# Performance work log

Hardware: AMD Instinct MI355X
Metric: run time of the kernel (lower is better)

Reference implementation:

```python
import jax, jax.numpy as jnp
import numpy as np
import math

D_MODEL = 96
D_STATE = 16
D_CONV = 3
D_INNER = 192          # expand=2 * d_model
DT_RANK = 6            # ceil(96/16)
K = 4                  # scan directions
B, H, W = 1, 64, 64


def setup_inputs() -> dict:
    key = jax.random.key(0)
    ks = jax.random.split(key, 10)
    x = jax.random.normal(ks[0], (B, H, W, D_MODEL), dtype=jnp.float32)
    in_proj_w = jax.random.normal(ks[1], (2 * D_INNER, D_MODEL), jnp.float32) / np.sqrt(D_MODEL)
    conv_w = jax.random.normal(ks[2], (D_CONV, D_CONV, 1, D_INNER), jnp.float32) * 0.1  # HWIO depthwise
    conv_b = jax.random.normal(ks[3], (D_INNER,), jnp.float32) * 0.01
    x_proj_w = jax.random.normal(ks[4], (K, DT_RANK + 2 * D_STATE, D_INNER), jnp.float32) / np.sqrt(D_INNER)
    dt_std = DT_RANK ** -0.5
    dt_w = jax.random.uniform(ks[5], (K, D_INNER, DT_RANK), jnp.float32, -dt_std, dt_std)
    # faithful dt bias init: dt ~ exp(U*(log(dt_max)-log(dt_min))+log(dt_min)), inverse-softplus
    dt = jnp.exp(jax.random.uniform(ks[6], (K, D_INNER), jnp.float32) * (math.log(0.1) - math.log(0.001)) + math.log(0.001))
    dt = jnp.clip(dt, 1e-4, None)
    dt_b = dt + jnp.log(-jnp.expm1(-dt))
    A_logs = jnp.tile(jnp.log(jnp.arange(1, D_STATE + 1, dtype=jnp.float32))[None, :], (K * D_INNER, 1))
    Ds = jnp.ones((K * D_INNER,), jnp.float32)
    ln_g = jnp.ones((D_INNER,), jnp.float32)
    ln_b = jnp.zeros((D_INNER,), jnp.float32)
    out_w = jax.random.normal(ks[7], (D_MODEL, D_INNER), jnp.float32) / np.sqrt(D_INNER)
    return dict(x=x, in_proj_w=in_proj_w, conv_w=conv_w, conv_b=conv_b, x_proj_w=x_proj_w,
                dt_w=dt_w, dt_b=dt_b, A_logs=A_logs, Ds=Ds, ln_g=ln_g, ln_b=ln_b, out_w=out_w)


def _silu(v):
    return v * jax.nn.sigmoid(v)


def _ss2d(x, in_proj_w, conv_w, conv_b, x_proj_w, dt_w, dt_b, A_logs, Ds, ln_g, ln_b, out_w):
    b, h, w, _ = x.shape
    L = h * w
    # in_proj, split x/z
    xz = jnp.einsum('bhwc,oc->bhwo', x, in_proj_w)
    x_, z = jnp.split(xz, 2, axis=-1)                              # (B,H,W,Di) each
    # depthwise 3x3 conv (SAME) + SiLU, NHWC
    xc = jax.lax.conv_general_dilated(x_, conv_w, (1, 1), 'SAME',
                                      dimension_numbers=('NHWC', 'HWIO', 'NHWC'),
                                      feature_group_count=D_INNER) + conv_b
    xc = _silu(xc)
    xd = xc.transpose(0, 3, 1, 2)                                   # (B,Di,H,W)
    x_row = xd.reshape(b, D_INNER, L)
    x_col = xd.transpose(0, 1, 3, 2).reshape(b, D_INNER, L)
    x_hwwh = jnp.stack([x_row, x_col], axis=1)                      # (B,2,Di,L)
    xs = jnp.concatenate([x_hwwh, jnp.flip(x_hwwh, axis=-1)], axis=1)  # (B,K,Di,L)
    # projections for dt / B / C
    x_dbl = jnp.einsum('bkdl,kcd->bkcl', xs, x_proj_w)
    dts = x_dbl[:, :, :DT_RANK]
    Bs = x_dbl[:, :, DT_RANK:DT_RANK + D_STATE]                     # (B,K,N,L)
    Cs = x_dbl[:, :, DT_RANK + D_STATE:]                            # (B,K,N,L)
    dts = jnp.einsum('bkrl,kdr->bkdl', dts, dt_w)
    delta = jax.nn.softplus(dts + dt_b[None, :, :, None])           # (B,K,Di,L)
    A = -jnp.exp(A_logs).reshape(K, D_INNER, D_STATE)
    # selective scan: h_l = exp(delta_l*A) h_{l-1} + delta_l*B_l*u_l ; y_l = C_l . h_l + D*u_l
    dA = jnp.exp(delta[..., None] * A[None, :, :, None, :])         # (B,K,Di,L,N)
    Bt = Bs.transpose(0, 1, 3, 2)                                   # (B,K,L,N)
    dBu = delta[..., None] * Bt[:, :, None] * xs[..., None]         # (B,K,Di,L,N)

    def comb(e1, e2):
        a1, b1 = e1
        a2, b2 = e2
        return a1 * a2, a2 * b1 + b2

    _, hstate = jax.lax.associative_scan(comb, (dA, dBu), axis=3)
    Ct = Cs.transpose(0, 1, 3, 2)                                   # (B,K,L,N)
    out_y = jnp.einsum('bkdln,bkln->bkdl', hstate, Ct) + Ds.reshape(K, D_INNER)[None, :, :, None] * xs
    y = out_y.sum(1).reshape(b, D_INNER, h, w).transpose(0, 2, 3, 1)  # (B,H,W,Di)
    # LayerNorm over channels
    mu = y.mean(-1, keepdims=True)
    var = y.var(-1, keepdims=True)
    y = (y - mu) * jax.lax.rsqrt(var + 1e-5) * ln_g + ln_b
    y = y * _silu(z)
    return jnp.einsum('bhwd,od->bhwo', y, out_w)


def reference(x, in_proj_w, conv_w, conv_b, x_proj_w, dt_w, dt_b, A_logs, Ds, ln_g, ln_b, out_w):
    return _ss2d(x, in_proj_w, conv_w, conv_b, x_proj_w, dt_w, dt_b, A_logs, Ds, ln_g, ln_b, out_w)
```

## Files before the change

kernel.cpp:

```cpp
#include <hip/hip_runtime.h>

#define L 4096
#define HH 64
#define WW 64
#define DM 96
#define DI 192
#define DSTATE 16
#define DTR 6
#define NC 38
#define NCP 40
#define KD 4
#define CHUNK 32
#define NCHUNK 128
#define NS 8
#define TL 8
#define LOG2E 1.44269504f
#define LN2   0.69314718f

__device__ __forceinline__ float silu_f(float v){ return v / (1.f + __expf(-v)); }
__device__ __forceinline__ float softplus_f(float v){
  float a = fabsf(v);
  float e = exp2f(-a * LOG2E);
  return fmaxf(v, 0.f) + LN2 * log2f(1.f + e);
}
__device__ __forceinline__ int spat(int k, int l){
  int ll = (k & 2) ? (L - 1 - l) : l;
  return (k & 1) ? (((ll & 63) << 6) | (ll >> 6)) : ll;
}

__global__ void k_prep(const float* __restrict__ ipw, const float* __restrict__ pw,
                       const float* __restrict__ ow,
                       float* __restrict__ ipwT, float* __restrict__ pwT,
                       float* __restrict__ owT){
  int i = blockIdx.x * 256 + threadIdx.x;
  if (i < 384*DM){ int o = i / DM, c = i % DM; ipwT[c*384 + o] = ipw[i]; }
  int j = i - 384*DM;
  if (j >= 0 && j < KD*NC*DI){
    int k = j / (NC*DI); int r = j % (NC*DI); int c = r / DI, d = r % DI;
    pwT[(k*DI + d)*NCP + c] = pw[j];
  }
  int m = i - 384*DM - KD*NC*DI;
  if (m >= 0 && m < DM*DI){ int o = m / DI, d = m % DI; owT[d*DM + o] = ow[m]; }
}

__global__ void k_inproj(const float* __restrict__ x, const float* __restrict__ wT,
                         float* __restrict__ xo, float* __restrict__ sz){
  int l0 = blockIdx.x * TL;
  int t  = threadIdx.x;
  __shared__ float xl[TL][DM];
  for (int j = t; j < TL*DM; j += 384) xl[j / DM][j % DM] = x[l0*DM + j];
  __syncthreads();
  float acc[TL];
  #pragma unroll
  for (int i = 0; i < TL; i++) acc[i] = 0.f;
  #pragma unroll 4
  for (int c = 0; c < DM; c++){
    float wv = wT[c*384 + t];
    #pragma unroll
    for (int i = 0; i < TL; i++) acc[i] += xl[i][c] * wv;
  }
  if (t < DI){
    #pragma unroll
    for (int i = 0; i < TL; i++) xo[(l0 + i)*DI + t] = acc[i];
  } else {
    int z = t - DI;
    #pragma unroll
    for (int i = 0; i < TL; i++) sz[(l0 + i)*DI + z] = silu_f(acc[i]);
  }
}

__global__ void k_conv(const float* __restrict__ xi, const float* __restrict__ cw,
                       const float* __restrict__ cb, float* __restrict__ xc){
  int idx = blockIdx.x * blockDim.x + threadIdx.x;
  if (idx >= L*DI) return;
  int d = idx % DI, l = idx / DI;
  int h = l >> 6, w = l & 63;
  float acc = cb[d];
  #pragma unroll
  for (int dy = 0; dy < 3; dy++){
    int hh = h + dy - 1;
    if (hh < 0 || hh >= HH) continue;
    #pragma unroll
    for (int dx = 0; dx < 3; dx++){
      int ww = w + dx - 1;
      if (ww < 0 || ww >= WW) continue;
      acc += xi[(hh*WW + ww)*DI + d] * cw[(dy*3 + dx)*DI + d];
    }
  }
  xc[idx] = silu_f(acc);
}

__global__ __launch_bounds__(384) void k_xs1(
    const float* __restrict__ xc, const float* __restrict__ pwT,
    const float* __restrict__ dtw, const float* __restrict__ dtb,
    const float* __restrict__ alogs,
    float* __restrict__ xdb, float* __restrict__ Pb, float* __restrict__ Gb){
  int k  = blockIdx.x >> 7;
  int ch = blockIdx.x & 127;
  int l0 = ch * CHUNK;
  int t  = threadIdx.x;
  __shared__ float sxc[CHUNK][DI + 1];
  __shared__ float sdt[CHUNK][8];
  __shared__ float sB[CHUNK][16];
  for (int j = t; j < CHUNK*DI; j += 384){
    int i = j / DI, dd = j % DI;
    sxc[i][dd] = xc[spat(k, l0 + i)*DI + dd];
  }
  __syncthreads();
  if (t < 320){
    int i = t / 10, cg = t % 10;
    const float4* pr4 = (const float4*)(pwT + k*DI*NCP) + cg;
    float4 a = make_float4(0.f, 0.f, 0.f, 0.f);
    #pragma unroll 8
    for (int dd = 0; dd < DI; dd++){
      float v = sxc[i][dd];
      float4 w = pr4[dd*10];
      a.x += v*w.x; a.y += v*w.y; a.z += v*w.z; a.w += v*w.w;
    }
    float av[4] = {a.x, a.y, a.z, a.w};
    int c0 = cg*4;
    #pragma unroll
    for (int q = 0; q < 4; q++){
      int c = c0 + q;
      if (c < NC){
        xdb[(size_t)(k*L + l0 + i)*NC + c] = av[q];
        if (c < DTR) sdt[i][c] = av[q];
        else if (c < DTR + DSTATE) sB[i][c - DTR] = av[q];
      }
    }
  }
  int d = t >> 1, half = t & 1;
  float wr[DTR];
  #pragma unroll
  for (int r = 0; r < DTR; r++) wr[r] = dtw[(k*DI + d)*DTR + r];
  float bb = dtb[k*DI + d];
  float A2[NS];
  const float* ap = alogs + (k*DI + d)*DSTATE + half*NS;
  #pragma unroll
  for (int j = 0; j < NS; j++) A2[j] = -__expf(ap[j]) * LOG2E;
  float P[NS], G[NS];
  #pragma unroll
  for (int j = 0; j < NS; j++){ P[j] = 1.f; G[j] = 0.f; }
  __syncthreads();
  #pragma unroll 8
  for (int i = 0; i < CHUNK; i++){
    float xval = sxc[i][d];
    float dv = bb;
    #pragma unroll
    for (int r = 0; r < DTR; r++) dv += wr[r] * sdt[i][r];
    dv = softplus_f(dv);
    float tv = dv * xval;
    float4 b0 = *(const float4*)&sB[i][half*8];
    float4 b1 = *(const float4*)&sB[i][half*8 + 4];
    float Bv[NS] = {b0.x,b0.y,b0.z,b0.w,b1.x,b1.y,b1.z,b1.w};
    #pragma unroll
    for (int j = 0; j < NS; j++){
      float dA = exp2f(dv * A2[j]);
      G[j] = dA * G[j] + tv * Bv[j];
      P[j] *= dA;
    }
  }
  size_t base = (size_t)(k*NCHUNK + ch)*DI*DSTATE + t*NS;
  ((float4*)(Pb + base))[0] = make_float4(P[0],P[1],P[2],P[3]);
  ((float4*)(Pb + base))[1] = make_float4(P[4],P[5],P[6],P[7]);
  ((float4*)(Gb + base))[0] = make_float4(G[0],G[1],G[2],G[3]);
  ((float4*)(Gb + base))[1] = make_float4(G[4],G[5],G[6],G[7]);
}

__global__ void k_scan2(const float* __restrict__ Pb, const float* __restrict__ Gb,
                        float* __restrict__ Hin){
  int k = blockIdx.x / DI;
  int d = blockIdx.x % DI;
  int c = threadIdx.x;
  float P[DSTATE], G[DSTATE];
  const float* Pp = Pb + ((size_t)(k*NCHUNK + c)*DI + d)*DSTATE;
  const float* Gp = Gb + ((size_t)(k*NCHUNK + c)*DI + d)*DSTATE;
  #pragma unroll
  for (int n = 0; n < DSTATE; n++){ P[n] = Pp[n]; G[n] = Gp[n]; }
  __shared__ float sP[NCHUNK][DSTATE + 1];
  __shared__ float sG[NCHUNK][DSTATE + 1];
  for (int off = 1; off < NCHUNK; off <<= 1){
    #pragma unroll
    for (int n = 0; n < DSTATE; n++){ sP[c][n] = P[n]; sG[c][n] = G[n]; }
    __syncthreads();
    if (c >= off){
      #pragma unroll
      for (int n = 0; n < DSTATE; n++){
        float a1 = sP[c - off][n], b1 = sG[c - off][n];
        G[n] = P[n]*b1 + G[n];
        P[n] = P[n]*a1;
      }
    }
    __syncthreads();
  }
  #pragma unroll
  for (int n = 0; n < DSTATE; n++) sG[c][n] = G[n];
  __syncthreads();
  float* Hp = Hin + ((size_t)(k*NCHUNK + c)*DI + d)*DSTATE;
  #pragma unroll
  for (int n = 0; n < DSTATE; n++) Hp[n] = (c == 0) ? 0.f : sG[c - 1][n];
}

__global__ __launch_bounds__(384) void k_scan3(
    const float* __restrict__ xdbl, const float* __restrict__ xc,
    const float* __restrict__ dtw, const float* __restrict__ dtb,
    const float* __restrict__ alogs, const float* __restrict__ Dsv,
    const float* __restrict__ Hin, float* __restrict__ oyT){
  int k  = blockIdx.x >> 7;
  int ch = blockIdx.x & 127;
  int l0 = ch * CHUNK;
  int t  = threadIdx.x;
  int d  = t >> 1, half = t & 1;
  __shared__ float sdt[CHUNK][8];
  __shared__ float sB[CHUNK][16];
  __shared__ float sC[CHUNK][16];
  __shared__ float sxc[CHUNK][DI];
  for (int j = t; j < CHUNK*NC; j += 384){
    int i = j / NC, c = j % NC;
    float v = xdbl[(size_t)(k*L + l0)*NC + j];
    if (c < DTR) sdt[i][c] = v;
    else if (c < DTR + DSTATE) sB[i][c - DTR] = v;
    else sC[i][c - DTR - DSTATE] = v;
  }
  for (int j = t; j < CHUNK*DI; j += 384){
    int i = j / DI, dd = j % DI;
    sxc[i][dd] = xc[spat(k, l0 + i)*DI + dd];
  }
  float wr[DTR];
  #pragma unroll
  for (int r = 0; r < DTR; r++) wr[r] = dtw[(k*DI + d)*DTR + r];
  float bb = dtb[k*DI + d];
  float A2[NS];
  const float* ap = alogs + (k*DI + d)*DSTATE + half*NS;
  #pragma unroll
  for (int j = 0; j < NS; j++) A2[j] = -__expf(ap[j]) * LOG2E;
  float h[NS];
  size_t hbase = (size_t)(k*NCHUNK + ch)*DI*DSTATE + t*NS;
  float4 h0 = ((const float4*)(Hin + hbase))[0];
  float4 h1 = ((const float4*)(Hin + hbase))[1];
  h[0]=h0.x; h[1]=h0.y; h[2]=h0.z; h[3]=h0.w;
  h[4]=h1.x; h[5]=h1.y; h[6]=h1.z; h[7]=h1.w;
  float Dv = Dsv[k*DI + d];
  __syncthreads();
  #pragma unroll 8
  for (int i = 0; i < CHUNK; i++){
    float xval = sxc[i][d];
    float dv = bb;
    #pragma unroll
    for (int r = 0; r < DTR; r++) dv += wr[r] * sdt[i][r];
    dv = softplus_f(dv);
    float tv = dv * xval;
    float4 b0 = *(const float4*)&sB[i][half*8];
    float4 b1 = *(const float4*)&sB[i][half*8 + 4];
    float4 c0 = *(const float4*)&sC[i][half*8];
    float4 c1 = *(const float4*)&sC[i][half*8 + 4];
    float Bv[NS] = {b0.x,b0.y,b0.z,b0.w,b1.x,b1.y,b1.z,b1.w};
    float Cv[NS] = {c0.x,c0.y,c0.z,c0.w,c1.x,c1.y,c1.z,c1.w};
    float y = (half == 0) ? Dv * xval : 0.f;
    #pragma unroll
    for (int j = 0; j < NS; j++){
      float dA = exp2f(dv * A2[j]);
      h[j] = dA * h[j] + tv * Bv[j];
      y += h[j] * Cv[j];
    }
    y += __shfl_xor(y, 1);
    if (half == 0) oyT[(size_t)(l0 + i)*KD*DI + k*DI + d] = y;
  }
}

__global__ void k_final(const float* __restrict__ oyT, const float* __restrict__ sz,
                        const float* __restrict__ g, const float* __restrict__ b,
                        const float* __restrict__ owT, float* __restrict__ out){
  int l = blockIdx.x, t = threadIdx.x;
  __shared__ float ym[DI];
  __shared__ float part[DI];
  __shared__ float red[6];
  float y = 0.f;
  #pragma unroll
  for (int k = 0; k < KD; k++) y += oyT[(size_t)l*KD*DI + k*DI + t];
  float s = y, s2 = y*y;
  #pragma unroll
  for (int off = 32; off; off >>= 1){ s += __shfl_down(s, off); s2 += __shfl_down(s2, off); }
  int wave = t >> 6, lane = t & 63;
  if (lane == 0){ red[wave] = s; red[3 + wave] = s2; }
  __syncthreads();
  float S  = red[0] + red[1] + red[2];
  float SQ = red[3] + red[4] + red[5];
  float mu  = S * (1.f/DI);
  float var = SQ * (1.f/DI) - mu*mu;
  float yn = (y - mu) * rsqrtf(var + 1e-5f) * g[t] + b[t];
  ym[t] = yn * sz[(size_t)l*DI + t];
  __syncthreads();
  int o  = (t < DM) ? t : (t - DM);
  int d0 = (t < DM) ? 0 : DM;
  float acc = 0.f;
  #pragma unroll 8
  for (int dd = 0; dd < DM; dd++){
    int d = d0 + dd;
    acc += ym[d] * owT[d*DM + o];
  }
  part[t] = acc;
  __syncthreads();
  if (t < DM) out[l*DM + t] = part[t] + part[DM + t];
}

extern "C" void kernel_launch(void* const* d_in, const int* in_sizes, int n_in,
                              void* d_out, int out_size, void* d_ws, size_t ws_size,
                              hipStream_t stream){
  const float* x   = (const float*)d_in[0];
  const float* ipw = (const float*)d_in[1];
  const float* cw  = (const float*)d_in[2];
  const float* cb  = (const float*)d_in[3];
  const float* pw  = (const float*)d_in[4];
  const float* dtw = (const float*)d_in[5];
  const float* dtb = (const float*)d_in[6];
  const float* alg = (const float*)d_in[7];
  const float* Dsv = (const float*)d_in[8];
  const float* lng = (const float*)d_in[9];
  const float* lnb = (const float*)d_in[10];
  const float* ow  = (const float*)d_in[11];
  float* out = (float*)d_out;

  float* ws    = (float*)d_ws;
  float* x_    = ws; ws += L*DI;
  float* sz    = ws; ws += L*DI;
  float* xc    = ws; ws += L*DI;
  float* xdb   = ws; ws += KD*L*NC;
  float* Pb    = ws; ws += KD*NCHUNK*DI*DSTATE;
  float* Gb    = ws; ws += KD*NCHUNK*DI*DSTATE;
  float* Hin   = ws; ws += KD*NCHUNK*DI*DSTATE;
  float* oyT   = ws; ws += (size_t)L*KD*DI;
  float* ipwT  = ws; ws += 384*DM;
  float* pwT   = ws; ws += KD*DI*NCP;
  float* owT   = ws; ws += DM*DI;

  k_prep<<<(384*DM + KD*NC*DI + DM*DI + 255)/256, 256, 0, stream>>>(ipw, pw, ow, ipwT, pwT, owT);
  k_inproj<<<L/TL, 384, 0, stream>>>(x, ipwT, x_, sz);
  k_conv<<<(L*DI + 383)/384, 384, 0, stream>>>(x_, cw, cb, xc);
  k_xs1<<<KD*NCHUNK, 384, 0, stream>>>(xc, pwT, dtw, dtb, alg, xdb, Pb, Gb);
  k_scan2<<<KD*DI, NCHUNK, 0, stream>>>(Pb, Gb, Hin);
  k_scan3<<<KD*NCHUNK, 384, 0, stream>>>(xdb, xc, dtw, dtb, alg, Dsv, Hin, oyT);
  k_final<<<L, DI, 0, stream>>>(oyT, sz, lng, lnb, owT, out);
}
```

Baseline: 211.1 us.

## Use finer chunks for first scan pass and pad x_dbl rows for vector stores

```diff
diff --git a/kernel.cpp b/kernel.cpp
--- a/kernel.cpp
+++ b/kernel.cpp
@@ -10,8 +10,10 @@
 #define NC 38
 #define NCP 40
 #define KD 4
-#define CHUNK 32
-#define NCHUNK 128
+#define CH1 16
+#define NCH1 256
+#define CH3 32
+#define NCH3 128
 #define NS 8
 #define TL 8
 #define LOG2E 1.44269504f
@@ -41,6 +43,11 @@
   }
   int m = i - 384*DM - KD*NC*DI;
   if (m >= 0 && m < DM*DI){ int o = m / DI, d = m % DI; owT[d*DM + o] = ow[m]; }
+  int p = m - DM*DI;
+  if (p >= 0 && p < KD*DI*2){
+    int kd = p >> 1, q = p & 1;
+    pwT[kd*NCP + NC + q] = 0.f;
+  }
 }
 
 __global__ void k_inproj(const float* __restrict__ x, const float* __restrict__ wT,
@@ -94,36 +101,42 @@
     const float* __restrict__ xc, const float* __restrict__ pwT,
     const float* __restrict__ dtw, const float* __restrict__ dtb,
     const float* __restrict__ alogs,
-    float* __restrict__ xdb, float* __restrict__ Pb, float* __restrict__ Gb){
-  int k  = blockIdx.x >> 7;
-  int ch = blockIdx.x & 127;
-  int l0 = ch * CHUNK;
+    float* __restrict__ xdbp, float* __restrict__ Pb, float* __restrict__ Gb){
+  int k  = blockIdx.x >> 8;
+  int ch = blockIdx.x & 255;
+  int l0 = ch * CH1;
   int t  = threadIdx.x;
-  __shared__ float sxc[CHUNK][DI + 1];
-  __shared__ float sdt[CHUNK][8];
-  __shared__ float sB[CHUNK][16];
-  for (int j = t; j < CHUNK*DI; j += 384){
+  __shared__ float sxc[CH1][DI + 1];
+  __shared__ float sdt[CH1][8];
+  __shared__ float sB[CH1][16];
+  for (int j = t; j < CH1*DI; j += 384){
     int i = j / DI, dd = j % DI;
     sxc[i][dd] = xc[spat(k, l0 + i)*DI + dd];
   }
   __syncthreads();
   if (t < 320){
-    int i = t / 10, cg = t % 10;
+    int i = t / 20, r = t % 20, cg = r >> 1, half2 = r & 1;
     const float4* pr4 = (const float4*)(pwT + k*DI*NCP) + cg;
     float4 a = make_float4(0.f, 0.f, 0.f, 0.f);
+    int dd0 = half2 * 96;
     #pragma unroll 8
-    for (int dd = 0; dd < DI; dd++){
+    for (int q = 0; q < 96; q++){
+      int dd = dd0 + q;
       float v = sxc[i][dd];
       float4 w = pr4[dd*10];
       a.x += v*w.x; a.y += v*w.y; a.z += v*w.z; a.w += v*w.w;
     }
-    float av[4] = {a.x, a.y, a.z, a.w};
-    int c0 = cg*4;
-    #pragma unroll
-    for (int q = 0; q < 4; q++){
-      int c = c0 + q;
-      if (c < NC){
-        xdb[(size_t)(k*L + l0 + i)*NC + c] = av[q];
+    a.x += __shfl_xor(a.x, 1);
+    a.y += __shfl_xor(a.y, 1);
+    a.z += __shfl_xor(a.z, 1);
+    a.w += __shfl_xor(a.w, 1);
+    if (half2 == 0){
+      *(float4*)&xdbp[(size_t)(k*L + l0 + i)*NCP + cg*4] = a;
+      float av[4] = {a.x, a.y, a.z, a.w};
+      int c0 = cg*4;
+      #pragma unroll
+      for (int q = 0; q < 4; q++){
+        int c = c0 + q;
         if (c < DTR) sdt[i][c] = av[q];
         else if (c < DTR + DSTATE) sB[i][c - DTR] = av[q];
       }
@@ -143,7 +156,7 @@
   for (int j = 0; j < NS; j++){ P[j] = 1.f; G[j] = 0.f; }
   __syncthreads();
   #pragma unroll 8
-  for (int i = 0; i < CHUNK; i++){
+  for (int i = 0; i < CH1; i++){
     float xval = sxc[i][d];
     float dv = bb;
     #pragma unroll
@@ -160,7 +173,7 @@
       P[j] *= dA;
     }
   }
-  size_t base = (size_t)(k*NCHUNK + ch)*DI*DSTATE + t*NS;
+  size_t base = (size_t)(k*NCH1 + ch)*DI*DSTATE + t*NS;
   ((float4*)(Pb + base))[0] = make_float4(P[0],P[1],P[2],P[3]);
   ((float4*)(Pb + base))[1] = make_float4(P[4],P[5],P[6],P[7]);
   ((float4*)(Gb + base))[0] = make_float4(G[0],G[1],G[2],G[3]);
@@ -173,13 +186,13 @@
   int d = blockIdx.x % DI;
   int c = threadIdx.x;
   float P[DSTATE], G[DSTATE];
-  const float* Pp = Pb + ((size_t)(k*NCHUNK + c)*DI + d)*DSTATE;
-  const float* Gp = Gb + ((size_t)(k*NCHUNK + c)*DI + d)*DSTATE;
+  const float* Pp = Pb + ((size_t)(k*NCH1 + c)*DI + d)*DSTATE;
+  const float* Gp = Gb + ((size_t)(k*NCH1 + c)*DI + d)*DSTATE;
   #pragma unroll
   for (int n = 0; n < DSTATE; n++){ P[n] = Pp[n]; G[n] = Gp[n]; }
-  __shared__ float sP[NCHUNK][DSTATE + 1];
-  __shared__ float sG[NCHUNK][DSTATE + 1];
-  for (int off = 1; off < NCHUNK; off <<= 1){
+  __shared__ float sP[NCH1][DSTATE + 1];
+  __shared__ float sG[NCH1][DSTATE + 1];
+  for (int off = 1; off < NCH1; off <<= 1){
     #pragma unroll
     for (int n = 0; n < DSTATE; n++){ sP[c][n] = P[n]; sG[c][n] = G[n]; }
     __syncthreads();
@@ -196,33 +209,33 @@
   #pragma unroll
   for (int n = 0; n < DSTATE; n++) sG[c][n] = G[n];
   __syncthreads();
-  float* Hp = Hin + ((size_t)(k*NCHUNK + c)*DI + d)*DSTATE;
+  float* Hp = Hin + ((size_t)(k*NCH1 + c)*DI + d)*DSTATE;
   #pragma unroll
   for (int n = 0; n < DSTATE; n++) Hp[n] = (c == 0) ? 0.f : sG[c - 1][n];
 }
 
 __global__ __launch_bounds__(384) void k_scan3(
-    const float* __restrict__ xdbl, const float* __restrict__ xc,
+    const float* __restrict__ xdbp, const float* __restrict__ xc,
     const float* __restrict__ dtw, const float* __restrict__ dtb,
     const float* __restrict__ alogs, const float* __restrict__ Dsv,
     const float* __restrict__ Hin, float* __restrict__ oyT){
   int k  = blockIdx.x >> 7;
   int ch = blockIdx.x & 127;
-  int l0 = ch * CHUNK;
+  int l0 = ch * CH3;
   int t  = threadIdx.x;
   int d  = t >> 1, half = t & 1;
-  __shared__ float sdt[CHUNK][8];
-  __shared__ float sB[CHUNK][16];
-  __shared__ float sC[CHUNK][16];
-  __shared__ float sxc[CHUNK][DI];
-  for (int j = t; j < CHUNK*NC; j += 384){
-    int i = j / NC, c = j % NC;
-    float v = xdbl[(size_t)(k*L + l0)*NC + j];
+  __shared__ float sdt[CH3][8];
+  __shared__ float sB[CH3][16];
+  __shared__ float sC[CH3][16];
+  __shared__ float sxc[CH3][DI];
+  for (int j = t; j < CH3*NCP; j += 384){
+    int i = j / NCP, c = j % NCP;
+    float v = xdbp[(size_t)(k*L + l0)*NCP + j];
     if (c < DTR) sdt[i][c] = v;
     else if (c < DTR + DSTATE) sB[i][c - DTR] = v;
-    else sC[i][c - DTR - DSTATE] = v;
-  }
-  for (int j = t; j < CHUNK*DI; j += 384){
+    else if (c < NC) sC[i][c - DTR - DSTATE] = v;
+  }
+  for (int j = t; j < CH3*DI; j += 384){
     int i = j / DI, dd = j % DI;
     sxc[i][dd] = xc[spat(k, l0 + i)*DI + dd];
   }
@@ -235,7 +248,7 @@
   #pragma unroll
   for (int j = 0; j < NS; j++) A2[j] = -__expf(ap[j]) * LOG2E;
   float h[NS];
-  size_t hbase = (size_t)(k*NCHUNK + ch)*DI*DSTATE + t*NS;
+  size_t hbase = (size_t)(k*NCH1 + 2*ch)*DI*DSTATE + t*NS;
   float4 h0 = ((const float4*)(Hin + hbase))[0];
   float4 h1 = ((const float4*)(Hin + hbase))[1];
   h[0]=h0.x; h[1]=h0.y; h[2]=h0.z; h[3]=h0.w;
@@ -243,7 +256,7 @@
   float Dv = Dsv[k*DI + d];
   __syncthreads();
   #pragma unroll 8
-  for (int i = 0; i < CHUNK; i++){
+  for (int i = 0; i < CH3; i++){
     float xval = sxc[i][d];
     float dv = bb;
     #pragma unroll
@@ -325,20 +338,21 @@
   float* x_    = ws; ws += L*DI;
   float* sz    = ws; ws += L*DI;
   float* xc    = ws; ws += L*DI;
-  float* xdb   = ws; ws += KD*L*NC;
-  float* Pb    = ws; ws += KD*NCHUNK*DI*DSTATE;
-  float* Gb    = ws; ws += KD*NCHUNK*DI*DSTATE;
-  float* Hin   = ws; ws += KD*NCHUNK*DI*DSTATE;
+  float* xdbp  = ws; ws += (size_t)KD*L*NCP;
+  float* Pb    = ws; ws += (size_t)KD*NCH1*DI*DSTATE;
+  float* Gb    = ws; ws += (size_t)KD*NCH1*DI*DSTATE;
+  float* Hin   = ws; ws += (size_t)KD*NCH1*DI*DSTATE;
   float* oyT   = ws; ws += (size_t)L*KD*DI;
   float* ipwT  = ws; ws += 384*DM;
   float* pwT   = ws; ws += KD*DI*NCP;
   float* owT   = ws; ws += DM*DI;
 
-  k_prep<<<(384*DM + KD*NC*DI + DM*DI + 255)/256, 256, 0, stream>>>(ipw, pw, ow, ipwT, pwT, owT);
+  int prep_tot = 384*DM + KD*NC*DI + DM*DI + KD*DI*2;
+  k_prep<<<(prep_tot + 255)/256, 256, 0, stream>>>(ipw, pw, ow, ipwT, pwT, owT);
   k_inproj<<<L/TL, 384, 0, stream>>>(x, ipwT, x_, sz);
   k_conv<<<(L*DI + 383)/384, 384, 0, stream>>>(x_, cw, cb, xc);
-  k_xs1<<<KD*NCHUNK, 384, 0, stream>>>(xc, pwT, dtw, dtb, alg, xdb, Pb, Gb);
-  k_scan2<<<KD*DI, NCHUNK, 0, stream>>>(Pb, Gb, Hin);
-  k_scan3<<<KD*NCHUNK, 384, 0, stream>>>(xdb, xc, dtw, dtb, alg, Dsv, Hin, oyT);
+  k_xs1<<<KD*NCH1, 384, 0, stream>>>(xc, pwT, dtw, dtb, alg, xdbp, Pb, Gb);
+  k_scan2<<<KD*DI, NCH1, 0, stream>>>(Pb, Gb, Hin);
+  k_scan3<<<KD*NCH3, 384, 0, stream>>>(xdbp, xc, dtw, dtb, alg, Dsv, Hin, oyT);
   k_final<<<L, DI, 0, stream>>>(oyT, sz, lng, lnb, owT, out);
 }
```

After: 222.1 us. +5.2%, slower.
